# Kernel tuning notes

Hardware: AMD Instinct MI355X
Metric: run time of the kernel (lower is better)

Reference implementation:

```python
import jax, jax.numpy as jnp
import numpy as np

NUM_HEADS = 8
DIM_HEAD = 64
SCALE = DIM_HEAD * NUM_HEADS  # q *= dim_head * num_heads, as in the source


def setup_inputs() -> dict:
    key = jax.random.key(0)
    k1, k2, k3, k4 = jax.random.split(key, 4)
    B, C, H, W = 8, 64, 32, 32
    x = jax.random.normal(k1, (B, C, H, W), dtype=jnp.float32)
    # 1x1 conv == matmul over channels; small init keeps post-scale logits sane
    w_qkv = jax.random.normal(k2, (3 * NUM_HEADS * DIM_HEAD, C), dtype=jnp.float32) * 0.02
    rel_h = jax.random.normal(k3, (2 * H - 1, DIM_HEAD), dtype=jnp.float32) * 0.02
    rel_w = jax.random.normal(k4, (2 * W - 1, DIM_HEAD), dtype=jnp.float32) * 0.02
    return {"x": x, "w_qkv": w_qkv, "rel_h": rel_h, "rel_w": rel_w}


def _rel_indices(H, W):
    # flattened 2D grid positions
    pos_y = np.repeat(np.arange(H), W)  # [HW]
    pos_x = np.tile(np.arange(W), H)    # [HW]
    rel_y = pos_y[None, :] - pos_y[:, None] + (H - 1)  # [HW, HW] in [0, 2H-2]
    rel_x = pos_x[None, :] - pos_x[:, None] + (W - 1)  # [HW, HW] in [0, 2W-2]
    return jnp.asarray(rel_y), jnp.asarray(rel_x)


def reference(x, w_qkv, rel_h, rel_w):
    B, C, H, W = x.shape
    n = H * W
    # 1x1 conv (bias=False) -> per-pixel matmul
    xf = x.reshape(B, C, n)                              # b c n
    qkv = jnp.einsum('oc,bcn->bon', w_qkv, xf)           # b (3 h d) n
    q, k, v = jnp.split(qkv, 3, axis=1)
    def to_heads(t):  # b (h d) n -> b h n d
        return t.reshape(B, NUM_HEADS, DIM_HEAD, n).transpose(0, 1, 3, 2)
    q, k, v = to_heads(q), to_heads(k), to_heads(v)
    q = q * SCALE  # scale applied before QK^T AND before pos bias (in-place in torch)

    sim = jnp.einsum('bhid,bhjd->bhij', q, k)            # [B, h, n, n]

    # relative position bias: q_i . rel_h[dy] + q_i . rel_w[dx]
    logits_h = jnp.einsum('bhid,rd->bhir', q, rel_h)     # [B, h, n, 2H-1]
    logits_w = jnp.einsum('bhid,rd->bhir', q, rel_w)     # [B, h, n, 2W-1]
    rel_y, rel_x = _rel_indices(H, W)                    # [n, n] each
    i_idx = jnp.arange(n)[:, None]                       # [n, 1]
    bias = logits_h[:, :, i_idx, rel_y] + logits_w[:, :, i_idx, rel_x]  # [B,h,n,n]

    attn = jax.nn.softmax(sim + bias, axis=-1)
    out = jnp.einsum('bhij,bhjd->bhid', attn, v)         # [B, h, n, d]
    out = out.transpose(0, 1, 3, 2).reshape(B, NUM_HEADS * DIM_HEAD, H, W)
    return out
```

## Files before the change

kernel.cpp:

```cpp
#include <hip/hip_runtime.h>
#include <hip/hip_bf16.h>
#include <hip/hip_fp16.h>

typedef _Float16 h8 __attribute__((ext_vector_type(8)));
typedef _Float16 h2 __attribute__((ext_vector_type(2)));
typedef unsigned short us8 __attribute__((ext_vector_type(8)));
typedef float f4 __attribute__((ext_vector_type(4)));
typedef float f16v __attribute__((ext_vector_type(16)));
typedef int i2v __attribute__((ext_vector_type(2)));

#define NH 8
#define DH 64
#define NPIX 1024
#define CIN 64
#define NBH 64
#define QSCALE (512.0f * 1.44269504f)
#define LOSCALE 2048.0f
#define INV_LOSCALE (1.0f / 2048.0f)
#define DTHR 12.0f

__device__ __forceinline__ void gload_lds16(const void* g, void* lds) {
  __builtin_amdgcn_global_load_lds(
      (const __attribute__((address_space(1))) void*)g,
      (__attribute__((address_space(3))) void*)lds, 16, 0, 0);
// ... 84 lines not shown
  f4 zf = {0.f, 0.f, 0.f, 0.f};
  f4 acc[2][4], cor[2][4];
  #pragma unroll
  for (int oi = 0; oi < 2; ++oi)
    #pragma unroll
    for (int pi = 0; pi < 4; ++pi) { acc[oi][pi] = zf; cor[oi][pi] = zf; }

  const int ob = w * 32;
  #pragma unroll
  for (int kh = 0; kh < 2; ++kh) {
    h8 ah[2], al[2], bh[4], bl[4];
    #pragma unroll
    for (int oi = 0; oi < 2; ++oi) {
      int orow = ob + ((c >> 2) << 3) + (c & 3) + oi * 4;
      int ch = (((kh * 4 + g) ^ (orow & 7)) << 4);
      ah[oi] = *(const h8*)(Wh + orow * 128 + ch);
      al[oi] = *(const h8*)(Wl + orow * 128 + ch);
    }
    #pragma unroll
    for (int pi = 0; pi < 4; ++pi) {
      int prow = pi * 16 + c;
      int ch = (((kh * 4 + g) ^ (prow & 7)) << 4);
      bh[pi] = *(const h8*)(Xh + prow * 128 + ch);
      bl[pi] = *(const h8*)(Xl + prow * 128 + ch);
    }
    __builtin_amdgcn_s_setprio(1);
    #pragma unroll
    for (int oi = 0; oi < 2; ++oi)
      #pragma unroll
      for (int pi = 0; pi < 4; ++pi) {
        acc[oi][pi] = __builtin_amdgcn_mfma_f32_16x16x32_f16(ah[oi], bh[pi], acc[oi][pi], 0, 0, 0);
        cor[oi][pi] = __builtin_amdgcn_mfma_f32_16x16x32_f16(ah[oi], bl[pi], cor[oi][pi], 0, 0, 0);
        cor[oi][pi] = __builtin_amdgcn_mfma_f32_16x16x32_f16(al[oi], bh[pi], cor[oi][pi], 0, 0, 0);
      }
    __builtin_amdgcn_s_setprio(0);
  }

  const int part = o0 >> 9;
  const float scl = part == 0 ? QSCALE : 1.0f;
  _Float16* dsth = part == 0 ? Qh : (part == 1 ? Kh : Vv);
  _Float16* dstl = part == 0 ? Ql : (part == 1 ? Kl : nullptr);

  __syncthreads();
  {
    const int chunk = 4 * w + g;
    #pragma unroll
    for (int pi = 0; pi < 4; ++pi) {
      int p = pi * 16 + c;
      h8 hv, lv;
      #pragma unroll
      for (int oi = 0; oi < 2; ++oi)
        #pragma unroll
        for (int reg = 0; reg < 4; ++reg) {
          float v = (acc[oi][pi][reg] + cor[oi][pi][reg] * INV_LOSCALE) * scl;
          _Float16 hh = (_Float16)v;
          hv[oi * 4 + reg] = hh;
          lv[oi * 4 + reg] = (_Float16)(v - (float)hh);
        }
      int byo = p * 256 + ((chunk ^ (p & 15)) << 4);
      *(h8*)(Thi + byo) = hv;
      if (dstl) *(h8*)(Tlo + byo) = lv;
    }
  }
  __syncthreads();
  #pragma unroll
  for (int it = 0; it < 4; ++it) {
    int task = tid + it * 256;
    int p = task >> 4;
    int ck = task & 15;
    int byo = p * 256 + ((ck ^ (p & 15)) << 4);
    int o = o0 + ck * 8;
    int h = (o >> 6) & 7;
    int d = o & 63;
    size_t off = (((size_t)(b * NH + h)) * NPIX + p0 + p) * DH + d;
    h8 v = *(const h8*)(Thi + byo);
    *(h8*)(dsth + off) = v;
    if (dstl) {
      h8 v2 = *(const h8*)(Tlo + byo);
      *(h8*)(dstl + off) = v2;
    }
  }
}

__global__ __launch_bounds__(256, 2) void attn_mfma(
    const _Float16* __restrict__ Qh, const _Float16* __restrict__ Ql,
    const _Float16* __restrict__ Kh, const _Float16* __restrict__ Kl,
    const _Float16* __restrict__ V,
    const float* __restrict__ rel_h, const float* __restrict__ rel_w,
    float* __restrict__ out) {
  __shared__ __align__(16) char SMem[57344];
  _Float16* LHc = (_Float16*)(SMem + 49152);
  _Float16* LWT = (_Float16*)(SMem + 32768);
  float* OT = (float*)SMem;

  const int tid = threadIdx.x;
  const int lane = tid & 63;
  const int w = tid >> 6;
  const int wu = __builtin_amdgcn_readfirstlane(w);
  const int c = lane & 15;
  const int g = lane >> 4;
  const int il = lane & 31;
  const int hi = lane >> 5;
  const int bx = blockIdx.x;
  const int bh = ((bx & 7) << 3) | ((bx >> 3) & 7);
  const int i0 = (bx >> 6) << 7;

  const _Float16* Qhg = Qh + (size_t)bh * NPIX * DH;
  const _Float16* Qlg = Ql + (size_t)bh * NPIX * DH;
  const _Float16* Khg = Kh + (size_t)bh * NPIX * DH;
  const _Float16* Klg = Kl + (size_t)bh * NPIX * DH;
  const _Float16* Vg  = V  + (size_t)bh * NPIX * DH;

  const h8* Qr0h = (const h8*)(Qhg + (size_t)(i0 + w * 32 + c) * DH);
  const h8* Qr0l = (const h8*)(Qlg + (size_t)(i0 + w * 32 + c) * DH);
  const h8* Qr1h = (const h8*)(Qhg + (size_t)(i0 + w * 32 + 16 + c) * DH);
  const h8* Qr1l = (const h8*)(Qlg + (size_t)(i0 + w * 32 + 16 + c) * DH);
  h8 q0h[2] = {Qr0h[g], Qr0h[4 + g]};
  h8 q0l[2] = {Qr0l[g], Qr0l[4 + g]};
  h8 q1h[2] = {Qr1h[g], Qr1h[4 + g]};
  h8 q1l[2] = {Qr1l[g], Qr1l[4 + g]};

  const int s0i = wu * 128 + lane;
  const int s1i = s0i + 64;
  const int ko0 = (s0i >> 3) * 128 + (((s0i & 7) ^ ((s0i >> 3) & 7)) << 4);
  const int ko1 = (s1i >> 3) * 128 + (((s1i & 7) ^ ((s1i >> 3) & 7)) << 4);

  #pragma unroll
  for (int it = 0; it < 2; ++it) {
    int task = tid + it * 256;
    int oct = task & 7, s = task >> 3;
    int ss = s < 63 ? s : 62;
    const float* sh = rel_h + (size_t)ss * DH + oct * 8;
    const float* sw = rel_w + (size_t)ss * DH + oct * 8;
    h8 hh, ww;
    #pragma unroll
    for (int e = 0; e < 8; ++e) {
      hh[e] = (_Float16)sh[e];
      ww[e] = (_Float16)sw[e];
    }
    int byo = s * 128 + ((oct ^ (s & 7)) << 4);
    *(h8*)(SMem + byo) = hh;
    *(h8*)(SMem + 16384 + byo) = ww;
  }
  __syncthreads();

  const int yi = (i0 + w * 32) >> 5;
  f4 zf = {0.f, 0.f, 0.f, 0.f};
  #pragma unroll
  for (int rs = 0; rs < 2; ++rs) {
    f4 lhD[4], lwD[4];
    #pragma unroll
    for (int st = 0; st < 4; ++st) { lhD[st] = zf; lwD[st] = zf; }
    #pragma unroll
    for (int kh = 0; kh < 2; ++kh) {
      h8 bq = rs ? q1h[kh] : q0h[kh];
      h8 bl = rs ? q1l[kh] : q0l[kh];
      #pragma unroll
      for (int st = 0; st < 4; ++st) {
        int srow = st * 16 + c;
        int chb = srow * 128 + (((kh * 4 + g) ^ (srow & 7)) << 4);
        h8 ra = *(const h8*)(SMem + chb);
        h8 wa = *(const h8*)(SMem + 16384 + chb);
        lhD[st] = __builtin_amdgcn_mfma_f32_16x16x32_f16(ra, bq, lhD[st], 0, 0, 0);
        lhD[st] = __builtin_amdgcn_mfma_f32_16x16x32_f16(ra, bl, lhD[st], 0, 0, 0);
        lwD[st] = __builtin_amdgcn_mfma_f32_16x16x32_f16(wa, bq, lwD[st], 0, 0, 0);
        lwD[st] = __builtin_amdgcn_mfma_f32_16x16x32_f16(wa, bl, lwD[st], 0, 0, 0);
      }
    }
    int lrow = w * 32 + rs * 16 + c;
    #pragma unroll
    for (int st = 0; st < 4; ++st)
      #pragma unroll
      for (int reg = 0; reg < 4; ++reg) {
        int s = st * 16 + 4 * g + reg;
        int k = s - 31 + yi;
        if (k >= 0 && k < 32)
          LHc[(k >> 1) * 256 + lrow * 2 + (k & 1)] = (_Float16)lhD[st][reg];
        LWT[lrow * 64 + s] = (_Float16)lwD[st][reg];
      }
  }
  __syncthreads();

  float lwp[16];
  {
    int r = w * 32 + il;
    #pragma unroll
    for (int reg = 0; reg < 16; ++reg) {
      int jl = (reg & 3) + 8 * (reg >> 2) + 4 * hi;
      lwp[reg] = (float)LWT[r * 64 + 31 + jl - il];
    }
  }
  const h8* Qmh = (const h8*)(Qhg + (size_t)(i0 + w * 32 + il) * DH);
  const h8* Qml = (const h8*)(Qlg + (size_t)(i0 + w * 32 + il) * DH);
  h8 qmh[4], qml[4];
  #pragma unroll
  for (int kb = 0; kb < 4; ++kb) {
    qmh[kb] = Qmh[2 * kb + hi];
    qml[kb] = Qml[2 * kb + hi];
  }
  __syncthreads();

  {
    gload_lds16((const char*)Khg + ko0, SMem + wu * 2048);
    gload_lds16((const char*)Khg + ko1, SMem + wu * 2048 + 1024);
    gload_lds16((const char*)Klg + ko0, SMem + 16384 + wu * 2048);
    gload_lds16((const char*)Klg + ko1, SMem + 16384 + wu * 2048 + 1024);
    int jp = tid & 31, dd = tid >> 5;
    const h8* vr = (const h8*)(Vg + (size_t)(2 * jp) * DH);
    h8 v0 = vr[dd], v1 = vr[8 + dd];
    us8 u0 = *(const us8*)&v0, u1 = *(const us8*)&v1;
    #pragma unroll
    for (int e = 0; e < 8; ++e) {
      int d = dd * 8 + e;
      unsigned int val = (unsigned int)u0[e] | ((unsigned int)u1[e] << 16);
      *(unsigned int*)(SMem + 32768 + d * 128 + (((jp >> 2) ^ (d & 7)) << 4) + (jp & 3) * 4) = val;
    }
  }
  __syncthreads();

  float m_s = -1e30f, lp = 0.f;
  f16v O0, O1;
  #pragma unroll
  for (int e = 0; e < 16; ++e) { O0[e] = 0.f; O1[e] = 0.f; }

  const int swl = (il & 7);
  int cur = 0;
  #pragma unroll 1
  for (int t = 0; t < 16; ++t) {
    char* Kc  = SMem + cur * 8192;
    char* KLc = SMem + 16384 + cur * 8192;
    char* Vc  = SMem + 32768 + cur * 8192;
    const int nxt = cur ^ 1;
    const bool pre = t < 15;
    const int jp = tid & 31, dd = tid >> 5;
    h8 v0 = {}, v1 = {};
    if (pre) {
      const char* kg  = (const char*)Khg + (size_t)(t + 1) * 8192;
      const char* klg = (const char*)Klg + (size_t)(t + 1) * 8192;
      gload_lds16(kg + ko0, SMem + nxt * 8192 + wu * 2048);
      gload_lds16(kg + ko1, SMem + nxt * 8192 + wu * 2048 + 1024);
      gload_lds16(klg + ko0, SMem + 16384 + nxt * 8192 + wu * 2048);
      gload_lds16(klg + ko1, SMem + 16384 + nxt * 8192 + wu * 2048 + 1024);
      const h8* vr = (const h8*)(Vg + (size_t)((t + 1) * 64 + 2 * jp) * DH);
      v0 = vr[dd];
      v1 = vr[8 + dd];
    }

    f16v S0, S1;
    #pragma unroll
    for (int e = 0; e < 16; ++e) { S0[e] = 0.f; S1[e] = 0.f; }
    #pragma unroll
    for (int kb = 0; kb < 4; ++kb) {
      int chb0 = il * 128 + (((2 * kb + hi) ^ swl) << 4);
      int chb1 = chb0 + 32 * 128;
      h8 a0h = *(const h8*)(Kc + chb0);
      h8 a0l = *(const h8*)(KLc + chb0);
      h8 a1h = *(const h8*)(Kc + chb1);
      h8 a1l = *(const h8*)(KLc + chb1);
      __builtin_amdgcn_s_setprio(1);
      S0 = __builtin_amdgcn_mfma_f32_32x32x16_f16(a0h, qmh[kb], S0, 0, 0, 0);
      S0 = __builtin_amdgcn_mfma_f32_32x32x16_f16(a0l, qmh[kb], S0, 0, 0, 0);
      S0 = __builtin_amdgcn_mfma_f32_32x32x16_f16(a0h, qml[kb], S0, 0, 0, 0);
      S1 = __builtin_amdgcn_mfma_f32_32x32x16_f16(a1h, qmh[kb], S1, 0, 0, 0);
      S1 = __builtin_amdgcn_mfma_f32_32x32x16_f16(a1l, qmh[kb], S1, 0, 0, 0);
      S1 = __builtin_amdgcn_mfma_f32_32x32x16_f16(a1h, qml[kb], S1, 0, 0, 0);
      __builtin_amdgcn_s_setprio(0);
    }

    h8 fr[4];
    {
      int r = w * 32 + il;
      h2 lhu = *(const h2*)(LHc + t * 256 + r * 2);
      float lh0 = (float)lhu[0], lh1 = (float)lhu[1];
      #pragma unroll
      for (int reg = 0; reg < 16; ++reg) {
        S0[reg] += lwp[reg] + lh0;
        S1[reg] += lwp[reg] + lh1;
      }
      float v8[8];
      #pragma unroll
      for (int e = 0; e < 8; ++e)
        v8[e] = fmaxf(fmaxf(S0[e], S0[e + 8]), fmaxf(S1[e], S1[e + 8]));
      float w0 = fmaxf(fmaxf(v8[0], v8[1]), fmaxf(v8[2], v8[3]));
      float w1 = fmaxf(fmaxf(v8[4], v8[5]), fmaxf(v8[6], v8[7]));
      float mx = fmaxf(w0, w1);
      mx = fmaxf(mx, __shfl_xor(mx, 32, 64));
      bool sk = mx <= m_s + DTHR;
      if (!__all(sk)) {
        float mn = fmaxf(m_s, mx);
        float corr = fexp2(m_s - mn);
        m_s = mn;
        lp *= corr;
        #pragma unroll
        for (int e = 0; e < 16; ++e) { O0[e] *= corr; O1[e] *= corr; }
      }
      float pv0[16], pv1[16];
      float sum = 0.f;
      #pragma unroll
      for (int e = 0; e < 16; ++e) {
        pv0[e] = fexp2(S0[e] - m_s);
        pv1[e] = fexp2(S1[e] - m_s);
        sum += pv0[e] + pv1[e];
      }
      lp += sum;
      #pragma unroll
      for (int jkb = 0; jkb < 4; ++jkb) {
        const float* pv = (jkb < 2) ? pv0 : pv1;
        int base = (jkb & 1) * 8;
        unsigned x01 = pk16(pv[base + 0], pv[base + 1]);
        unsigned x23 = pk16(pv[base + 2], pv[base + 3]);
        unsigned y01 = pk16(pv[base + 4], pv[base + 5]);
        unsigned y23 = pk16(pv[base + 6], pv[base + 7]);
        i2v r1 = __builtin_amdgcn_permlane32_swap((int)x01, (int)y01, false, false);
        i2v r2 = __builtin_amdgcn_permlane32_swap((int)x23, (int)y23, false, false);
        union { unsigned u[4]; h8 h; } fu;
        fu.u[0] = (unsigned)r1[0];
        fu.u[1] = (unsigned)r2[0];
        fu.u[2] = (unsigned)r1[1];
        fu.u[3] = (unsigned)r2[1];
        fr[jkb] = fu.h;
      }
    }

    #pragma unroll
    for (int jkb = 0; jkb < 4; ++jkb) {
      int och = (((2 * jkb + hi) ^ swl) << 4);
      __builtin_amdgcn_s_setprio(1);
      h8 av0 = *(const h8*)(Vc + il * 128 + och);
      h8 av1 = *(const h8*)(Vc + (32 + il) * 128 + och);
      O0 = __builtin_amdgcn_mfma_f32_32x32x16_f16(av0, fr[jkb], O0, 0, 0, 0);
      O1 = __builtin_amdgcn_mfma_f32_32x32x16_f16(av1, fr[jkb], O1, 0, 0, 0);
      __builtin_amdgcn_s_setprio(0);
    }

    if (pre) {
      us8 u0 = *(const us8*)&v0, u1 = *(const us8*)&v1;
      char* Vn = SMem + 32768 + nxt * 8192;
      #pragma unroll
      for (int e = 0; e < 8; ++e) {
        int d = dd * 8 + e;
        unsigned int val = (unsigned int)u0[e] | ((unsigned int)u1[e] << 16);
        *(unsigned int*)(Vn + d * 128 + (((jp >> 2) ^ (d & 7)) << 4) + (jp & 3) * 4) = val;
      }
    }
    __syncthreads();
    cur = nxt;
  }

  float lt = lp + __shfl_xor(lp, 32, 64);
  float rr = __builtin_amdgcn_rcpf(lt);
  {
    int r = w * 32 + il;
    #pragma unroll
    for (int reg = 0; reg < 16; ++reg) {
      int dl = (reg & 3) + 8 * (reg >> 2) + 4 * hi;
      int d0 = dl;
      int d1 = 32 + dl;
      OT[d0 * 128 + (r ^ ((d0 & 7) << 3))] = O0[reg] * rr;
      OT[d1 * 128 + (r ^ ((d1 & 7) << 3))] = O1[reg] * rr;
    }
  }
  __syncthreads();
  #pragma unroll
  for (int it = 0; it < 8; ++it) {
    int task = tid + it * 256;
    int rq = task & 31, d = task >> 5;
    f4 vv = *(const f4*)&OT[d * 128 + ((rq * 4) ^ ((d & 7) << 3))];
    *(f4*)(out + (((size_t)bh * 64 + d) << 10) + i0 + rq * 4) = vv;
  }
}

extern "C" void kernel_launch(void* const* d_in, const int* in_sizes, int n_in,
                              void* d_out, int out_size, void* d_ws, size_t ws_size,
                              hipStream_t stream) {
  const float* x  = (const float*)d_in[0];
  const float* wq = (const float*)d_in[1];
  const float* rh = (const float*)d_in[2];
  const float* rw = (const float*)d_in[3];
  float* out = (float*)d_out;

  const size_t sz = (size_t)NBH * NPIX * DH;
  _Float16* Qh = (_Float16*)d_ws;
  _Float16* Ql = Qh + sz;
  _Float16* Kh = Ql + sz;
  _Float16* Kl = Kh + sz;
  _Float16* V  = Kl + sz;

  qkv_mfma<<<dim3(12, 16, 8), 256, 0, stream>>>(x, wq, Qh, Ql, Kh, Kl, V);
  attn_mfma<<<dim3(512), 256, 0, stream>>>(Qh, Ql, Kh, Kl, V, rh, rw, out);
}
```

Baseline: 72.10 us.

## Software-pipeline QK^T of next tile with softmax and PV of current tile

Restructures the attention main loop into a two-stage software pipeline. The QK^T MFMAs for tile t+1 are issued before the softmax and PV of tile t, using two sets of score accumulators (SA/SB) and a loop unrolled by two over explicit named LDS buffers. This lets MFMA work overlap the exp/max/pack ALU work. The prologue now prefetches two K tiles, the V register prefetch is held in persistent registers, and the row-sum reduction uses four partial sums. The extra 32 accumulator registers per lane raise register pressure under launch_bounds(256,2), which risks spills or lower occupancy.

Result: slower. 73.68 us (+2.2%).

```diff
diff --git a/kernel.cpp b/kernel.cpp
--- a/kernel.cpp
+++ b/kernel.cpp
@@ -200,6 +200,12 @@
   _Float16* LHc = (_Float16*)(SMem + 49152);
   _Float16* LWT = (_Float16*)(SMem + 32768);
   float* OT = (float*)SMem;
+  char* kb0 = SMem;
+  char* kb1 = SMem + 8192;
+  char* klb0 = SMem + 16384;
+  char* klb1 = SMem + 24576;
+  char* vb0 = SMem + 32768;
+  char* vb1 = SMem + 40960;
 
   const int tid = threadIdx.x;
   const int lane = tid & 63;
@@ -209,9 +215,11 @@
   const int g = lane >> 4;
   const int il = lane & 31;
   const int hi = lane >> 5;
+  const int jp = tid & 31, dd = tid >> 5;
   const int bx = blockIdx.x;
   const int bh = ((bx & 7) << 3) | ((bx >> 3) & 7);
   const int i0 = (bx >> 6) << 7;
+  const int swl = (il & 7);
 
   const _Float16* Qhg = Qh + (size_t)bh * NPIX * DH;
   const _Float16* Qlg = Ql + (size_t)bh * NPIX * DH;
@@ -308,55 +316,15 @@
   }
   __syncthreads();
 
-  {
-    gload_lds16((const char*)Khg + ko0, SMem + wu * 2048);
-    gload_lds16((const char*)Khg + ko1, SMem + wu * 2048 + 1024);
-    gload_lds16((const char*)Klg + ko0, SMem + 16384 + wu * 2048);
-    gload_lds16((const char*)Klg + ko1, SMem + 16384 + wu * 2048 + 1024);
-    int jp = tid & 31, dd = tid >> 5;
-    const h8* vr = (const h8*)(Vg + (size_t)(2 * jp) * DH);
-    h8 v0 = vr[dd], v1 = vr[8 + dd];
-    us8 u0 = *(const us8*)&v0, u1 = *(const us8*)&v1;
-    #pragma unroll
-    for (int e = 0; e < 8; ++e) {
-      int d = dd * 8 + e;
-      unsigned int val = (unsigned int)u0[e] | ((unsigned int)u1[e] << 16);
-      *(unsigned int*)(SMem + 32768 + d * 128 + (((jp >> 2) ^ (d & 7)) << 4) + (jp & 3) * 4) = val;
-    }
-  }
-  __syncthreads();
-
   float m_s = -1e30f, lp = 0.f;
-  f16v O0, O1;
+  f16v O0, O1, SA0, SA1, SB0, SB1;
   #pragma unroll
   for (int e = 0; e < 16; ++e) { O0[e] = 0.f; O1[e] = 0.f; }
-
-  const int swl = (il & 7);
-  int cur = 0;
-  #pragma unroll 1
-  for (int t = 0; t < 16; ++t) {
-    char* Kc  = SMem + cur * 8192;
-    char* KLc = SMem + 16384 + cur * 8192;
-    char* Vc  = SMem + 32768 + cur * 8192;
-    const int nxt = cur ^ 1;
-    const bool pre = t < 15;
-    const int jp = tid & 31, dd = tid >> 5;
-    h8 v0 = {}, v1 = {};
-    if (pre) {
-      const char* kg  = (const char*)Khg + (size_t)(t + 1) * 8192;
-      const char* klg = (const char*)Klg + (size_t)(t + 1) * 8192;
-      gload_lds16(kg + ko0, SMem + nxt * 8192 + wu * 2048);
-      gload_lds16(kg + ko1, SMem + nxt * 8192 + wu * 2048 + 1024);
-      gload_lds16(klg + ko0, SMem + 16384 + nxt * 8192 + wu * 2048);
-      gload_lds16(klg + ko1, SMem + 16384 + nxt * 8192 + wu * 2048 + 1024);
-      const h8* vr = (const h8*)(Vg + (size_t)((t + 1) * 64 + 2 * jp) * DH);
-      v0 = vr[dd];
-      v1 = vr[8 + dd];
-    }
-
-    f16v S0, S1;
-    #pragma unroll
-    for (int e = 0; e < 16; ++e) { S0[e] = 0.f; S1[e] = 0.f; }
+  h8 vr0, vr1;
+
+  auto qk = [&](const char* Kc, const char* KLc, f16v& T0, f16v& T1) {
+    #pragma unroll
+    for (int e = 0; e < 16; ++e) { T0[e] = 0.f; T1[e] = 0.f; }
     #pragma unroll
     for (int kb = 0; kb < 4; ++kb) {
       int chb0 = il * 128 + (((2 * kb + hi) ^ swl) << 4);
@@ -366,70 +334,77 @@
       h8 a1h = *(const h8*)(Kc + chb1);
       h8 a1l = *(const h8*)(KLc + chb1);
       __builtin_amdgcn_s_setprio(1);
-      S0 = __builtin_amdgcn_mfma_f32_32x32x16_f16(a0h, qmh[kb], S0, 0, 0, 0);
-      S0 = __builtin_amdgcn_mfma_f32_32x32x16_f16(a0l, qmh[kb], S0, 0, 0, 0);
-      S0 = __builtin_amdgcn_mfma_f32_32x32x16_f16(a0h, qml[kb], S0, 0, 0, 0);
-      S1 = __builtin_amdgcn_mfma_f32_32x32x16_f16(a1h, qmh[kb], S1, 0, 0, 0);
-      S1 = __builtin_amdgcn_mfma_f32_32x32x16_f16(a1l, qmh[kb], S1, 0, 0, 0);
-      S1 = __builtin_amdgcn_mfma_f32_32x32x16_f16(a1h, qml[kb], S1, 0, 0, 0);
+      T0 = __builtin_amdgcn_mfma_f32_32x32x16_f16(a0h, qmh[kb], T0, 0, 0, 0);
+      T0 = __builtin_amdgcn_mfma_f32_32x32x16_f16(a0l, qmh[kb], T0, 0, 0, 0);
+      T0 = __builtin_amdgcn_mfma_f32_32x32x16_f16(a0h, qml[kb], T0, 0, 0, 0);
+      T1 = __builtin_amdgcn_mfma_f32_32x32x16_f16(a1h, qmh[kb], T1, 0, 0, 0);
+      T1 = __builtin_amdgcn_mfma_f32_32x32x16_f16(a1l, qmh[kb], T1, 0, 0, 0);
+      T1 = __builtin_amdgcn_mfma_f32_32x32x16_f16(a1h, qml[kb], T1, 0, 0, 0);
       __builtin_amdgcn_s_setprio(0);
     }
-
-    h8 fr[4];
-    {
-      int r = w * 32 + il;
-      h2 lhu = *(const h2*)(LHc + t * 256 + r * 2);
-      float lh0 = (float)lhu[0], lh1 = (float)lhu[1];
+  };
+
+  auto finish = [&](int t, f16v& S0, f16v& S1, h8* fr) {
+    int r = w * 32 + il;
+    h2 lhu = *(const h2*)(LHc + t * 256 + r * 2);
+    float lh0 = (float)lhu[0], lh1 = (float)lhu[1];
+    #pragma unroll
+    for (int reg = 0; reg < 16; ++reg) {
+      S0[reg] += lwp[reg] + lh0;
+      S1[reg] += lwp[reg] + lh1;
+    }
+    float v8[8];
+    #pragma unroll
+    for (int e = 0; e < 8; ++e)
+      v8[e] = fmaxf(fmaxf(S0[e], S0[e + 8]), fmaxf(S1[e], S1[e + 8]));
+    float w0 = fmaxf(fmaxf(v8[0], v8[1]), fmaxf(v8[2], v8[3]));
+    float w1 = fmaxf(fmaxf(v8[4], v8[5]), fmaxf(v8[6], v8[7]));
+    float mx = fmaxf(w0, w1);
+    mx = fmaxf(mx, __shfl_xor(mx, 32, 64));
+    bool sk = mx <= m_s + DTHR;
+    if (!__all(sk)) {
+      float mn = fmaxf(m_s, mx);
+      float corr = fexp2(m_s - mn);
+      m_s = mn;
+      lp *= corr;
       #pragma unroll
-      for (int reg = 0; reg < 16; ++reg) {
-        S0[reg] += lwp[reg] + lh0;
-        S1[reg] += lwp[reg] + lh1;
-      }
-      float v8[8];
-      #pragma unroll
-      for (int e = 0; e < 8; ++e)
-        v8[e] = fmaxf(fmaxf(S0[e], S0[e + 8]), fmaxf(S1[e], S1[e + 8]));
-      float w0 = fmaxf(fmaxf(v8[0], v8[1]), fmaxf(v8[2], v8[3]));
-      float w1 = fmaxf(fmaxf(v8[4], v8[5]), fmaxf(v8[6], v8[7]));
-      float mx = fmaxf(w0, w1);
-      mx = fmaxf(mx, __shfl_xor(mx, 32, 64));
-      bool sk = mx <= m_s + DTHR;
-      if (!__all(sk)) {
-        float mn = fmaxf(m_s, mx);
-        float corr = fexp2(m_s - mn);
-        m_s = mn;
-        lp *= corr;
-        #pragma unroll
-        for (int e = 0; e < 16; ++e) { O0[e] *= corr; O1[e] *= corr; }
-      }
-      float pv0[16], pv1[16];
-      float sum = 0.f;
-      #pragma unroll
-      for (int e = 0; e < 16; ++e) {
-        pv0[e] = fexp2(S0[e] - m_s);
-        pv1[e] = fexp2(S1[e] - m_s);
-        sum += pv0[e] + pv1[e];
-      }
-      lp += sum;
-      #pragma unroll
-      for (int jkb = 0; jkb < 4; ++jkb) {
-        const float* pv = (jkb < 2) ? pv0 : pv1;
-        int base = (jkb & 1) * 8;
-        unsigned x01 = pk16(pv[base + 0], pv[base + 1]);
-        unsigned x23 = pk16(pv[base + 2], pv[base + 3]);
-        unsigned y01 = pk16(pv[base + 4], pv[base + 5]);
-        unsigned y23 = pk16(pv[base + 6], pv[base + 7]);
-        i2v r1 = __builtin_amdgcn_permlane32_swap((int)x01, (int)y01, false, false);
-        i2v r2 = __builtin_amdgcn_permlane32_swap((int)x23, (int)y23, false, false);
-        union { unsigned u[4]; h8 h; } fu;
-        fu.u[0] = (unsigned)r1[0];
-        fu.u[1] = (unsigned)r2[0];
-        fu.u[2] = (unsigned)r1[1];
-        fu.u[3] = (unsigned)r2[1];
-        fr[jkb] = fu.h;
-      }
-    }
-
+      for (int e = 0; e < 16; ++e) { O0[e] *= corr; O1[e] *= corr; }
+    }
+    float pv0[16], pv1[16];
+    #pragma unroll
+    for (int e = 0; e < 16; ++e) {
+      pv0[e] = fexp2(S0[e] - m_s);
+      pv1[e] = fexp2(S1[e] - m_s);
+    }
+    f4 ps = zf;
+    #pragma unroll
+    for (int e = 0; e < 16; e += 4) {
+      ps[0] += pv0[e] + pv1[e];
+      ps[1] += pv0[e + 1] + pv1[e + 1];
+      ps[2] += pv0[e + 2] + pv1[e + 2];
+      ps[3] += pv0[e + 3] + pv1[e + 3];
+    }
+    lp += (ps[0] + ps[1]) + (ps[2] + ps[3]);
+    #pragma unroll
+    for (int jkb = 0; jkb < 4; ++jkb) {
+      const float* pv = (jkb < 2) ? pv0 : pv1;
+      int base = (jkb & 1) * 8;
+      unsigned x01 = pk16(pv[base + 0], pv[base + 1]);
+      unsigned x23 = pk16(pv[base + 2], pv[base + 3]);
+      unsigned y01 = pk16(pv[base + 4], pv[base + 5]);
+      unsigned y23 = pk16(pv[base + 6], pv[base + 7]);
+      i2v r1 = __builtin_amdgcn_permlane32_swap((int)x01, (int)y01, false, false);
+      i2v r2 = __builtin_amdgcn_permlane32_swap((int)x23, (int)y23, false, false);
+      union { unsigned u[4]; h8 h; } fu;
+      fu.u[0] = (unsigned)r1[0];
+      fu.u[1] = (unsigned)r2[0];
+      fu.u[2] = (unsigned)r1[1];
+      fu.u[3] = (unsigned)r2[1];
+      fr[jkb] = fu.h;
+    }
+  };
+
+  auto pv_step = [&](const char* Vc, const h8* fr) {
     #pragma unroll
     for (int jkb = 0; jkb < 4; ++jkb) {
       int och = (((2 * jkb + hi) ^ swl) << 4);
@@ -440,19 +415,87 @@
       O1 = __builtin_amdgcn_mfma_f32_32x32x16_f16(av1, fr[jkb], O1, 0, 0, 0);
       __builtin_amdgcn_s_setprio(0);
     }
-
-    if (pre) {
-      us8 u0 = *(const us8*)&v0, u1 = *(const us8*)&v1;
-      char* Vn = SMem + 32768 + nxt * 8192;
-      #pragma unroll
-      for (int e = 0; e < 8; ++e) {
-        int d = dd * 8 + e;
-        unsigned int val = (unsigned int)u0[e] | ((unsigned int)u1[e] << 16);
-        *(unsigned int*)(Vn + d * 128 + (((jp >> 2) ^ (d & 7)) << 4) + (jp & 3) * 4) = val;
-      }
-    }
-    __syncthreads();
-    cur = nxt;
+  };
+
+  auto vwrite = [&](char* vb) {
+    us8 u0 = *(const us8*)&vr0, u1 = *(const us8*)&vr1;
+    #pragma unroll
+    for (int e = 0; e < 8; ++e) {
+      int d = dd * 8 + e;
+      unsigned val = (unsigned)u0[e] | ((unsigned)u1[e] << 16);
+      *(unsigned*)(vb + d * 128 + (((jp >> 2) ^ (d & 7)) << 4) + (jp & 3) * 4) = val;
+    }
+  };
+
+  {
+    gload_lds16((const char*)Khg + ko0, kb0 + wu * 2048);
+    gload_lds16((const char*)Khg + ko1, kb0 + wu * 2048 + 1024);
+    gload_lds16((const char*)Klg + ko0, klb0 + wu * 2048);
+    gload_lds16((const char*)Klg + ko1, klb0 + wu * 2048 + 1024);
+    gload_lds16((const char*)Khg + 8192 + ko0, kb1 + wu * 2048);
+    gload_lds16((const char*)Khg + 8192 + ko1, kb1 + wu * 2048 + 1024);
+    gload_lds16((const char*)Klg + 8192 + ko0, klb1 + wu * 2048);
+    gload_lds16((const char*)Klg + 8192 + ko1, klb1 + wu * 2048 + 1024);
+    const h8* vrp = (const h8*)(Vg + (size_t)(2 * jp) * DH);
+    vr0 = vrp[dd];
+    vr1 = vrp[8 + dd];
+  }
+  __syncthreads();
+  vwrite(vb0);
+  {
+    const h8* vrp = (const h8*)(Vg + (size_t)(64 + 2 * jp) * DH);
+    vr0 = vrp[dd];
+    vr1 = vrp[8 + dd];
+  }
+  qk(kb0, klb0, SA0, SA1);
+  __syncthreads();
+
+  #pragma unroll 1
+  for (int tp = 0; tp < 8; ++tp) {
+    {
+      const int t = 2 * tp;
+      if (t < 14) {
+        const char* kg  = (const char*)Khg + (size_t)(t + 2) * 8192;
+        const char* klg = (const char*)Klg + (size_t)(t + 2) * 8192;
+        gload_lds16(kg + ko0, kb0 + wu * 2048);
+        gload_lds16(kg + ko1, kb0 + wu * 2048 + 1024);
+        gload_lds16(klg + ko0, klb0 + wu * 2048);
+        gload_lds16(klg + ko1, klb0 + wu * 2048 + 1024);
+      }
+      if (t < 15) vwrite(vb1);
+      if (t < 14) {
+        const h8* vrp = (const h8*)(Vg + (size_t)((t + 2) * 64 + 2 * jp) * DH);
+        vr0 = vrp[dd];
+        vr1 = vrp[8 + dd];
+      }
+      if (t < 15) qk(kb1, klb1, SB0, SB1);
+      h8 fr[4];
+      finish(t, SA0, SA1, fr);
+      pv_step(vb0, fr);
+      __syncthreads();
+    }
+    {
+      const int t = 2 * tp + 1;
+      if (t < 14) {
+        const char* kg  = (const char*)Khg + (size_t)(t + 2) * 8192;
+        const char* klg = (const char*)Klg + (size_t)(t + 2) * 8192;
+        gload_lds16(kg + ko0, kb1 + wu * 2048);
+        gload_lds16(kg + ko1, kb1 + wu * 2048 + 1024);
+        gload_lds16(klg + ko0, klb1 + wu * 2048);
+        gload_lds16(klg + ko1, klb1 + wu * 2048 + 1024);
+      }
+      if (t < 15) vwrite(vb0);
+      if (t < 14) {
+        const h8* vrp = (const h8*)(Vg + (size_t)((t + 2) * 64 + 2 * jp) * DH);
+        vr0 = vrp[dd];
+        vr1 = vrp[8 + dd];
+      }
+      if (t < 15) qk(kb0, klb0, SA0, SA1);
+      h8 fr[4];
+      finish(t, SB0, SB1, fr);
+      pv_step(vb1, fr);
+      __syncthreads();
+    }
   }
 
   float lt = lp + __shfl_xor(lp, 32, 64);
```

## Keep row-bias terms in registers, shrink LDS, raise occupancy, unroll KV loop

Applied to the files above, without the earlier changes.

The per-row height-bias values move out of a dedicated LDS region and into 16 packed registers per lane, loaded once before the main loop. LDS per block drops from 56 KB to 48 KB and the launch bound rises to 3 blocks per CU. The 16-step key/value loop is fully unrolled so buffer offsets become compile-time constants, and the row-sum reduction is split into four partial accumulators. More waves can hide memory latency, but the register budget at 3 blocks per CU is tighter, so the compiler may spill.

Result: no change. 71.76 us (-0.5%).

```diff
diff --git a/kernel.cpp b/kernel.cpp
--- a/kernel.cpp
+++ b/kernel.cpp
@@ -190,15 +190,15 @@
   }
 }
 
-__global__ __launch_bounds__(256, 2) void attn_mfma(
+__global__ __launch_bounds__(256, 3) void attn_mfma(
     const _Float16* __restrict__ Qh, const _Float16* __restrict__ Ql,
     const _Float16* __restrict__ Kh, const _Float16* __restrict__ Kl,
     const _Float16* __restrict__ V,
     const float* __restrict__ rel_h, const float* __restrict__ rel_w,
     float* __restrict__ out) {
-  __shared__ __align__(16) char SMem[57344];
-  _Float16* LHc = (_Float16*)(SMem + 49152);
-  _Float16* LWT = (_Float16*)(SMem + 32768);
+  __shared__ __align__(16) char SMem[49152];
+  _Float16* LWT = (_Float16*)SMem;
+  _Float16* LHt = (_Float16*)(SMem + 16384);
   float* OT = (float*)SMem;
 
   const int tid = threadIdx.x;
@@ -209,9 +209,11 @@
   const int g = lane >> 4;
   const int il = lane & 31;
   const int hi = lane >> 5;
+  const int jp = tid & 31, dd = tid >> 5;
   const int bx = blockIdx.x;
   const int bh = ((bx & 7) << 3) | ((bx >> 3) & 7);
   const int i0 = (bx >> 6) << 7;
+  const int swl = (il & 7);
 
   const _Float16* Qhg = Qh + (size_t)bh * NPIX * DH;
   const _Float16* Qlg = Ql + (size_t)bh * NPIX * DH;
@@ -247,8 +249,8 @@
       ww[e] = (_Float16)sw[e];
     }
     int byo = s * 128 + ((oct ^ (s & 7)) << 4);
-    *(h8*)(SMem + byo) = hh;
-    *(h8*)(SMem + 16384 + byo) = ww;
+    *(h8*)(SMem + 32768 + byo) = hh;
+    *(h8*)(SMem + 40960 + byo) = ww;
   }
   __syncthreads();
 
@@ -267,8 +269,8 @@
       for (int st = 0; st < 4; ++st) {
         int srow = st * 16 + c;
         int chb = srow * 128 + (((kh * 4 + g) ^ (srow & 7)) << 4);
-        h8 ra = *(const h8*)(SMem + chb);
-        h8 wa = *(const h8*)(SMem + 16384 + chb);
+        h8 ra = *(const h8*)(SMem + 32768 + chb);
+        h8 wa = *(const h8*)(SMem + 40960 + chb);
         lhD[st] = __builtin_amdgcn_mfma_f32_16x16x32_f16(ra, bq, lhD[st], 0, 0, 0);
         lhD[st] = __builtin_amdgcn_mfma_f32_16x16x32_f16(ra, bl, lhD[st], 0, 0, 0);
         lwD[st] = __builtin_amdgcn_mfma_f32_16x16x32_f16(wa, bq, lwD[st], 0, 0, 0);
@@ -282,14 +284,14 @@
       for (int reg = 0; reg < 4; ++reg) {
         int s = st * 16 + 4 * g + reg;
         int k = s - 31 + yi;
-        if (k >= 0 && k < 32)
-          LHc[(k >> 1) * 256 + lrow * 2 + (k & 1)] = (_Float16)lhD[st][reg];
+        if (k >= 0 && k < 32) LHt[lrow * 32 + k] = (_Float16)lhD[st][reg];
         LWT[lrow * 64 + s] = (_Float16)lwD[st][reg];
       }
   }
   __syncthreads();
 
   float lwp[16];
+  unsigned lhreg[16];
   {
     int r = w * 32 + il;
     #pragma unroll
@@ -297,6 +299,9 @@
       int jl = (reg & 3) + 8 * (reg >> 2) + 4 * hi;
       lwp[reg] = (float)LWT[r * 64 + 31 + jl - il];
     }
+    #pragma unroll
+    for (int t = 0; t < 16; ++t)
+      lhreg[t] = *(const unsigned*)(LHt + r * 32 + 2 * t);
   }
   const h8* Qmh = (const h8*)(Qhg + (size_t)(i0 + w * 32 + il) * DH);
   const h8* Qml = (const h8*)(Qlg + (size_t)(i0 + w * 32 + il) * DH);
@@ -313,15 +318,14 @@
     gload_lds16((const char*)Khg + ko1, SMem + wu * 2048 + 1024);
     gload_lds16((const char*)Klg + ko0, SMem + 16384 + wu * 2048);
     gload_lds16((const char*)Klg + ko1, SMem + 16384 + wu * 2048 + 1024);
-    int jp = tid & 31, dd = tid >> 5;
     const h8* vr = (const h8*)(Vg + (size_t)(2 * jp) * DH);
     h8 v0 = vr[dd], v1 = vr[8 + dd];
     us8 u0 = *(const us8*)&v0, u1 = *(const us8*)&v1;
     #pragma unroll
     for (int e = 0; e < 8; ++e) {
       int d = dd * 8 + e;
-      unsigned int val = (unsigned int)u0[e] | ((unsigned int)u1[e] << 16);
-      *(unsigned int*)(SMem + 32768 + d * 128 + (((jp >> 2) ^ (d & 7)) << 4) + (jp & 3) * 4) = val;
+      unsigned val = (unsigned)u0[e] | ((unsigned)u1[e] << 16);
+      *(unsigned*)(SMem + 32768 + d * 128 + (((jp >> 2) ^ (d & 7)) << 4) + (jp & 3) * 4) = val;
     }
   }
   __syncthreads();
@@ -331,24 +335,22 @@
   #pragma unroll
   for (int e = 0; e < 16; ++e) { O0[e] = 0.f; O1[e] = 0.f; }
 
-  const int swl = (il & 7);
-  int cur = 0;
-  #pragma unroll 1
+  #pragma unroll
   for (int t = 0; t < 16; ++t) {
-    char* Kc  = SMem + cur * 8192;
-    char* KLc = SMem + 16384 + cur * 8192;
-    char* Vc  = SMem + 32768 + cur * 8192;
-    const int nxt = cur ^ 1;
-    const bool pre = t < 15;
-    const int jp = tid & 31, dd = tid >> 5;
+    char* Kc  = SMem + (t & 1) * 8192;
+    char* KLc = SMem + 16384 + (t & 1) * 8192;
+    char* Vc  = SMem + 32768 + (t & 1) * 8192;
+    char* Kn  = SMem + ((t + 1) & 1) * 8192;
+    char* KLn = SMem + 16384 + ((t + 1) & 1) * 8192;
+    char* Vn  = SMem + 32768 + ((t + 1) & 1) * 8192;
     h8 v0 = {}, v1 = {};
-    if (pre) {
+    if (t < 15) {
       const char* kg  = (const char*)Khg + (size_t)(t + 1) * 8192;
       const char* klg = (const char*)Klg + (size_t)(t + 1) * 8192;
-      gload_lds16(kg + ko0, SMem + nxt * 8192 + wu * 2048);
-      gload_lds16(kg + ko1, SMem + nxt * 8192 + wu * 2048 + 1024);
-      gload_lds16(klg + ko0, SMem + 16384 + nxt * 8192 + wu * 2048);
-      gload_lds16(klg + ko1, SMem + 16384 + nxt * 8192 + wu * 2048 + 1024);
+      gload_lds16(kg + ko0, Kn + wu * 2048);
+      gload_lds16(kg + ko1, Kn + wu * 2048 + 1024);
+      gload_lds16(klg + ko0, KLn + wu * 2048);
+      gload_lds16(klg + ko1, KLn + wu * 2048 + 1024);
       const h8* vr = (const h8*)(Vg + (size_t)((t + 1) * 64 + 2 * jp) * DH);
       v0 = vr[dd];
       v1 = vr[8 + dd];
@@ -377,9 +379,9 @@
 
     h8 fr[4];
     {
-      int r = w * 32 + il;
-      h2 lhu = *(const h2*)(LHc + t * 256 + r * 2);
-      float lh0 = (float)lhu[0], lh1 = (float)lhu[1];
+      union { unsigned u; h2 h; } lu;
+      lu.u = lhreg[t];
+      float lh0 = (float)lu.h[0], lh1 = (float)lu.h[1];
       #pragma unroll
       for (int reg = 0; reg < 16; ++reg) {
         S0[reg] += lwp[reg] + lh0;
@@ -403,14 +405,20 @@
         for (int e = 0; e < 16; ++e) { O0[e] *= corr; O1[e] *= corr; }
       }
       float pv0[16], pv1[16];
-      float sum = 0.f;
       #pragma unroll
       for (int e = 0; e < 16; ++e) {
         pv0[e] = fexp2(S0[e] - m_s);
         pv1[e] = fexp2(S1[e] - m_s);
-        sum += pv0[e] + pv1[e];
-      }
-      lp += sum;
+      }
+      f4 ps = zf;
+      #pragma unroll
+      for (int e = 0; e < 16; e += 4) {
+        ps[0] += pv0[e] + pv1[e];
+        ps[1] += pv0[e + 1] + pv1[e + 1];
+        ps[2] += pv0[e + 2] + pv1[e + 2];
+        ps[3] += pv0[e + 3] + pv1[e + 3];
+      }
+      lp += (ps[0] + ps[1]) + (ps[2] + ps[3]);
       #pragma unroll
       for (int jkb = 0; jkb < 4; ++jkb) {
         const float* pv = (jkb < 2) ? pv0 : pv1;
@@ -441,18 +449,16 @@
       __builtin_amdgcn_s_setprio(0);
     }
 
-    if (pre) {
+    if (t < 15) {
       us8 u0 = *(const us8*)&v0, u1 = *(const us8*)&v1;
-      char* Vn = SMem + 32768 + nxt * 8192;
       #pragma unroll
       for (int e = 0; e < 8; ++e) {
         int d = dd * 8 + e;
-        unsigned int val = (unsigned int)u0[e] | ((unsigned int)u1[e] << 16);
-        *(unsigned int*)(Vn + d * 128 + (((jp >> 2) ^ (d & 7)) << 4) + (jp & 3) * 4) = val;
+        unsigned val = (unsigned)u0[e] | ((unsigned)u1[e] << 16);
+        *(unsigned*)(Vn + d * 128 + (((jp >> 2) ^ (d & 7)) << 4) + (jp & 3) * 4) = val;
       }
     }
     __syncthreads();
-    cur = nxt;
   }
 
   float lt = lp + __shfl_xor(lp, 32, 64);
```

## Split key loop across two wave groups per block and merge softmax partials

Applied to the files above, without the earlier changes.

Doubles the attention block to 512 threads and splits the 16 key/value tiles between two groups of four waves, each keeping its own online-softmax state. The partial max, sum and output accumulators are exchanged through shared memory and merged at the end. Each group now single-buffers its K/V tiles with extra barriers instead of double-buffering. This aims to raise wave occupancy and halve the serial loop length, at the cost of more synchronisation, a merge step and less load/compute overlap per group.

Measured after the change: 80.30 us. +11.4%, slower.

```diff
diff --git a/kernel.cpp b/kernel.cpp
--- a/kernel.cpp
+++ b/kernel.cpp
@@ -190,7 +190,7 @@
   }
 }
 
-__global__ __launch_bounds__(256, 2) void attn_mfma(
+__global__ __launch_bounds__(512) void attn_mfma(
     const _Float16* __restrict__ Qh, const _Float16* __restrict__ Ql,
     const _Float16* __restrict__ Kh, const _Float16* __restrict__ Kl,
     const _Float16* __restrict__ V,
@@ -199,19 +199,28 @@
   __shared__ __align__(16) char SMem[57344];
   _Float16* LHc = (_Float16*)(SMem + 49152);
   _Float16* LWT = (_Float16*)(SMem + 32768);
+  float* EX = (float*)SMem;
   float* OT = (float*)SMem;
 
   const int tid = threadIdx.x;
   const int lane = tid & 63;
-  const int w = tid >> 6;
-  const int wu = __builtin_amdgcn_readfirstlane(w);
+  const int wu = tid >> 6;
+  const int lw = wu & 3;
+  const int grp = wu >> 2;
   const int c = lane & 15;
   const int g = lane >> 4;
   const int il = lane & 31;
   const int hi = lane >> 5;
+  const int gtid = tid & 255;
+  const int jp = gtid & 31, dd = gtid >> 5;
   const int bx = blockIdx.x;
   const int bh = ((bx & 7) << 3) | ((bx >> 3) & 7);
   const int i0 = (bx >> 6) << 7;
+  const int swl = (il & 7);
+
+  char* KHb = SMem + grp * 8192;
+  char* KLb = SMem + 16384 + grp * 8192;
+  char* VBb = SMem + 32768 + grp * 8192;
 
   const _Float16* Qhg = Qh + (size_t)bh * NPIX * DH;
   const _Float16* Qlg = Ql + (size_t)bh * NPIX * DH;
@@ -219,24 +228,13 @@
   const _Float16* Klg = Kl + (size_t)bh * NPIX * DH;
   const _Float16* Vg  = V  + (size_t)bh * NPIX * DH;
 
-  const h8* Qr0h = (const h8*)(Qhg + (size_t)(i0 + w * 32 + c) * DH);
-  const h8* Qr0l = (const h8*)(Qlg + (size_t)(i0 + w * 32 + c) * DH);
-  const h8* Qr1h = (const h8*)(Qhg + (size_t)(i0 + w * 32 + 16 + c) * DH);
-  const h8* Qr1l = (const h8*)(Qlg + (size_t)(i0 + w * 32 + 16 + c) * DH);
-  h8 q0h[2] = {Qr0h[g], Qr0h[4 + g]};
-  h8 q0l[2] = {Qr0l[g], Qr0l[4 + g]};
-  h8 q1h[2] = {Qr1h[g], Qr1h[4 + g]};
-  h8 q1l[2] = {Qr1l[g], Qr1l[4 + g]};
-
-  const int s0i = wu * 128 + lane;
+  const int s0i = lw * 128 + lane;
   const int s1i = s0i + 64;
   const int ko0 = (s0i >> 3) * 128 + (((s0i & 7) ^ ((s0i >> 3) & 7)) << 4);
   const int ko1 = (s1i >> 3) * 128 + (((s1i & 7) ^ ((s1i >> 3) & 7)) << 4);
 
-  #pragma unroll
-  for (int it = 0; it < 2; ++it) {
-    int task = tid + it * 256;
-    int oct = task & 7, s = task >> 3;
+  {
+    int oct = tid & 7, s = tid >> 3;
     int ss = s < 63 ? s : 62;
     const float* sh = rel_h + (size_t)ss * DH + oct * 8;
     const float* sw = rel_w + (size_t)ss * DH + oct * 8;
@@ -252,54 +250,64 @@
   }
   __syncthreads();
 
-  const int yi = (i0 + w * 32) >> 5;
   f4 zf = {0.f, 0.f, 0.f, 0.f};
-  #pragma unroll
-  for (int rs = 0; rs < 2; ++rs) {
-    f4 lhD[4], lwD[4];
-    #pragma unroll
-    for (int st = 0; st < 4; ++st) { lhD[st] = zf; lwD[st] = zf; }
-    #pragma unroll
-    for (int kh = 0; kh < 2; ++kh) {
-      h8 bq = rs ? q1h[kh] : q0h[kh];
-      h8 bl = rs ? q1l[kh] : q0l[kh];
-      #pragma unroll
-      for (int st = 0; st < 4; ++st) {
-        int srow = st * 16 + c;
-        int chb = srow * 128 + (((kh * 4 + g) ^ (srow & 7)) << 4);
-        h8 ra = *(const h8*)(SMem + chb);
-        h8 wa = *(const h8*)(SMem + 16384 + chb);
-        lhD[st] = __builtin_amdgcn_mfma_f32_16x16x32_f16(ra, bq, lhD[st], 0, 0, 0);
-        lhD[st] = __builtin_amdgcn_mfma_f32_16x16x32_f16(ra, bl, lhD[st], 0, 0, 0);
-        lwD[st] = __builtin_amdgcn_mfma_f32_16x16x32_f16(wa, bq, lwD[st], 0, 0, 0);
-        lwD[st] = __builtin_amdgcn_mfma_f32_16x16x32_f16(wa, bl, lwD[st], 0, 0, 0);
-      }
-    }
-    int lrow = w * 32 + rs * 16 + c;
-    #pragma unroll
-    for (int st = 0; st < 4; ++st)
-      #pragma unroll
-      for (int reg = 0; reg < 4; ++reg) {
-        int s = st * 16 + 4 * g + reg;
-        int k = s - 31 + yi;
-        if (k >= 0 && k < 32)
-          LHc[(k >> 1) * 256 + lrow * 2 + (k & 1)] = (_Float16)lhD[st][reg];
-        LWT[lrow * 64 + s] = (_Float16)lwD[st][reg];
-      }
+  if (grp == 0) {
+    const h8* Qr0h = (const h8*)(Qhg + (size_t)(i0 + lw * 32 + c) * DH);
+    const h8* Qr0l = (const h8*)(Qlg + (size_t)(i0 + lw * 32 + c) * DH);
+    const h8* Qr1h = (const h8*)(Qhg + (size_t)(i0 + lw * 32 + 16 + c) * DH);
+    const h8* Qr1l = (const h8*)(Qlg + (size_t)(i0 + lw * 32 + 16 + c) * DH);
+    h8 q0h[2] = {Qr0h[g], Qr0h[4 + g]};
+    h8 q0l[2] = {Qr0l[g], Qr0l[4 + g]};
+    h8 q1h[2] = {Qr1h[g], Qr1h[4 + g]};
+    h8 q1l[2] = {Qr1l[g], Qr1l[4 + g]};
+    const int yi = (i0 + lw * 32) >> 5;
+    #pragma unroll
+    for (int rs = 0; rs < 2; ++rs) {
+      f4 lhD[4], lwD[4];
+      #pragma unroll
+      for (int st = 0; st < 4; ++st) { lhD[st] = zf; lwD[st] = zf; }
+      #pragma unroll
+      for (int kh = 0; kh < 2; ++kh) {
+        h8 bq = rs ? q1h[kh] : q0h[kh];
+        h8 bl = rs ? q1l[kh] : q0l[kh];
+        #pragma unroll
+        for (int st = 0; st < 4; ++st) {
+          int srow = st * 16 + c;
+          int chb = srow * 128 + (((kh * 4 + g) ^ (srow & 7)) << 4);
+          h8 ra = *(const h8*)(SMem + chb);
+          h8 wa = *(const h8*)(SMem + 16384 + chb);
+          lhD[st] = __builtin_amdgcn_mfma_f32_16x16x32_f16(ra, bq, lhD[st], 0, 0, 0);
+          lhD[st] = __builtin_amdgcn_mfma_f32_16x16x32_f16(ra, bl, lhD[st], 0, 0, 0);
+          lwD[st] = __builtin_amdgcn_mfma_f32_16x16x32_f16(wa, bq, lwD[st], 0, 0, 0);
+          lwD[st] = __builtin_amdgcn_mfma_f32_16x16x32_f16(wa, bl, lwD[st], 0, 0, 0);
+        }
+      }
+      int lrow = lw * 32 + rs * 16 + c;
+      #pragma unroll
+      for (int st = 0; st < 4; ++st)
+        #pragma unroll
+        for (int reg = 0; reg < 4; ++reg) {
+          int s = st * 16 + 4 * g + reg;
+          int k = s - 31 + yi;
+          if (k >= 0 && k < 32)
+            LHc[(k >> 1) * 256 + lrow * 2 + (k & 1)] = (_Float16)lhD[st][reg];
+          LWT[lrow * 64 + s] = (_Float16)lwD[st][reg];
+        }
+    }
   }
   __syncthreads();
 
   float lwp[16];
   {
-    int r = w * 32 + il;
+    int r = lw * 32 + il;
     #pragma unroll
     for (int reg = 0; reg < 16; ++reg) {
       int jl = (reg & 3) + 8 * (reg >> 2) + 4 * hi;
       lwp[reg] = (float)LWT[r * 64 + 31 + jl - il];
     }
   }
-  const h8* Qmh = (const h8*)(Qhg + (size_t)(i0 + w * 32 + il) * DH);
-  const h8* Qml = (const h8*)(Qlg + (size_t)(i0 + w * 32 + il) * DH);
+  const h8* Qmh = (const h8*)(Qhg + (size_t)(i0 + lw * 32 + il) * DH);
+  const h8* Qml = (const h8*)(Qlg + (size_t)(i0 + lw * 32 + il) * DH);
   h8 qmh[4], qml[4];
   #pragma unroll
   for (int kb = 0; kb < 4; ++kb) {
@@ -308,20 +316,20 @@
   }
   __syncthreads();
 
-  {
-    gload_lds16((const char*)Khg + ko0, SMem + wu * 2048);
-    gload_lds16((const char*)Khg + ko1, SMem + wu * 2048 + 1024);
-    gload_lds16((const char*)Klg + ko0, SMem + 16384 + wu * 2048);
-    gload_lds16((const char*)Klg + ko1, SMem + 16384 + wu * 2048 + 1024);
-    int jp = tid & 31, dd = tid >> 5;
-    const h8* vr = (const h8*)(Vg + (size_t)(2 * jp) * DH);
+  const int tg0 = grp << 3;
+  {
+    gload_lds16((const char*)Khg + (size_t)tg0 * 8192 + ko0, KHb + lw * 2048);
+    gload_lds16((const char*)Khg + (size_t)tg0 * 8192 + ko1, KHb + lw * 2048 + 1024);
+    gload_lds16((const char*)Klg + (size_t)tg0 * 8192 + ko0, KLb + lw * 2048);
+    gload_lds16((const char*)Klg + (size_t)tg0 * 8192 + ko1, KLb + lw * 2048 + 1024);
+    const h8* vr = (const h8*)(Vg + (size_t)(tg0 * 64 + 2 * jp) * DH);
     h8 v0 = vr[dd], v1 = vr[8 + dd];
     us8 u0 = *(const us8*)&v0, u1 = *(const us8*)&v1;
     #pragma unroll
     for (int e = 0; e < 8; ++e) {
       int d = dd * 8 + e;
-      unsigned int val = (unsigned int)u0[e] | ((unsigned int)u1[e] << 16);
-      *(unsigned int*)(SMem + 32768 + d * 128 + (((jp >> 2) ^ (d & 7)) << 4) + (jp & 3) * 4) = val;
+      unsigned val = (unsigned)u0[e] | ((unsigned)u1[e] << 16);
+      *(unsigned*)(VBb + d * 128 + (((jp >> 2) ^ (d & 7)) << 4) + (jp & 3) * 4) = val;
     }
   }
   __syncthreads();
@@ -331,25 +339,13 @@
   #pragma unroll
   for (int e = 0; e < 16; ++e) { O0[e] = 0.f; O1[e] = 0.f; }
 
-  const int swl = (il & 7);
-  int cur = 0;
   #pragma unroll 1
-  for (int t = 0; t < 16; ++t) {
-    char* Kc  = SMem + cur * 8192;
-    char* KLc = SMem + 16384 + cur * 8192;
-    char* Vc  = SMem + 32768 + cur * 8192;
-    const int nxt = cur ^ 1;
-    const bool pre = t < 15;
-    const int jp = tid & 31, dd = tid >> 5;
+  for (int t = 0; t < 8; ++t) {
+    const int tg = tg0 + t;
+    const bool pre = t < 7;
     h8 v0 = {}, v1 = {};
     if (pre) {
-      const char* kg  = (const char*)Khg + (size_t)(t + 1) * 8192;
-      const char* klg = (const char*)Klg + (size_t)(t + 1) * 8192;
-      gload_lds16(kg + ko0, SMem + nxt * 8192 + wu * 2048);
-      gload_lds16(kg + ko1, SMem + nxt * 8192 + wu * 2048 + 1024);
-      gload_lds16(klg + ko0, SMem + 16384 + nxt * 8192 + wu * 2048);
-      gload_lds16(klg + ko1, SMem + 16384 + nxt * 8192 + wu * 2048 + 1024);
-      const h8* vr = (const h8*)(Vg + (size_t)((t + 1) * 64 + 2 * jp) * DH);
+      const h8* vr = (const h8*)(Vg + (size_t)((tg + 1) * 64 + 2 * jp) * DH);
       v0 = vr[dd];
       v1 = vr[8 + dd];
     }
@@ -361,10 +357,10 @@
     for (int kb = 0; kb < 4; ++kb) {
       int chb0 = il * 128 + (((2 * kb + hi) ^ swl) << 4);
       int chb1 = chb0 + 32 * 128;
-      h8 a0h = *(const h8*)(Kc + chb0);
-      h8 a0l = *(const h8*)(KLc + chb0);
-      h8 a1h = *(const h8*)(Kc + chb1);
-      h8 a1l = *(const h8*)(KLc + chb1);
+      h8 a0h = *(const h8*)(KHb + chb0);
+      h8 a0l = *(const h8*)(KLb + chb0);
+      h8 a1h = *(const h8*)(KHb + chb1);
+      h8 a1l = *(const h8*)(KLb + chb1);
       __builtin_amdgcn_s_setprio(1);
       S0 = __builtin_amdgcn_mfma_f32_32x32x16_f16(a0h, qmh[kb], S0, 0, 0, 0);
       S0 = __builtin_amdgcn_mfma_f32_32x32x16_f16(a0l, qmh[kb], S0, 0, 0, 0);
@@ -377,8 +373,8 @@
 
     h8 fr[4];
     {
-      int r = w * 32 + il;
-      h2 lhu = *(const h2*)(LHc + t * 256 + r * 2);
+      int r = lw * 32 + il;
+      h2 lhu = *(const h2*)(LHc + tg * 256 + r * 2);
       float lh0 = (float)lhu[0], lh1 = (float)lhu[1];
       #pragma unroll
       for (int reg = 0; reg < 16; ++reg) {
@@ -403,14 +399,20 @@
         for (int e = 0; e < 16; ++e) { O0[e] *= corr; O1[e] *= corr; }
       }
       float pv0[16], pv1[16];
-      float sum = 0.f;
       #pragma unroll
       for (int e = 0; e < 16; ++e) {
         pv0[e] = fexp2(S0[e] - m_s);
         pv1[e] = fexp2(S1[e] - m_s);
-        sum += pv0[e] + pv1[e];
-      }
-      lp += sum;
+      }
+      f4 ps = zf;
+      #pragma unroll
+      for (int e = 0; e < 16; e += 4) {
+        ps[0] += pv0[e] + pv1[e];
+        ps[1] += pv0[e + 1] + pv1[e + 1];
+        ps[2] += pv0[e + 2] + pv1[e + 2];
+        ps[3] += pv0[e + 3] + pv1[e + 3];
+      }
+      lp += (ps[0] + ps[1]) + (ps[2] + ps[3]);
       #pragma unroll
       for (int jkb = 0; jkb < 4; ++jkb) {
         const float* pv = (jkb < 2) ? pv0 : pv1;
@@ -429,49 +431,76 @@
         fr[jkb] = fu.h;
       }
     }
+    __syncthreads();
+    if (pre) {
+      const char* kg  = (const char*)Khg + (size_t)(tg + 1) * 8192;
+      const char* klg = (const char*)Klg + (size_t)(tg + 1) * 8192;
+      gload_lds16(kg + ko0, KHb + lw * 2048);
+      gload_lds16(kg + ko1, KHb + lw * 2048 + 1024);
+      gload_lds16(klg + ko0, KLb + lw * 2048);
+      gload_lds16(klg + ko1, KLb + lw * 2048 + 1024);
+    }
 
     #pragma unroll
     for (int jkb = 0; jkb < 4; ++jkb) {
       int och = (((2 * jkb + hi) ^ swl) << 4);
       __builtin_amdgcn_s_setprio(1);
-      h8 av0 = *(const h8*)(Vc + il * 128 + och);
-      h8 av1 = *(const h8*)(Vc + (32 + il) * 128 + och);
+      h8 av0 = *(const h8*)(VBb + il * 128 + och);
+      h8 av1 = *(const h8*)(VBb + (32 + il) * 128 + och);
       O0 = __builtin_amdgcn_mfma_f32_32x32x16_f16(av0, fr[jkb], O0, 0, 0, 0);
       O1 = __builtin_amdgcn_mfma_f32_32x32x16_f16(av1, fr[jkb], O1, 0, 0, 0);
       __builtin_amdgcn_s_setprio(0);
     }
-
+    __syncthreads();
     if (pre) {
       us8 u0 = *(const us8*)&v0, u1 = *(const us8*)&v1;
-      char* Vn = SMem + 32768 + nxt * 8192;
       #pragma unroll
       for (int e = 0; e < 8; ++e) {
         int d = dd * 8 + e;
-        unsigned int val = (unsigned int)u0[e] | ((unsigned int)u1[e] << 16);
-        *(unsigned int*)(Vn + d * 128 + (((jp >> 2) ^ (d & 7)) << 4) + (jp & 3) * 4) = val;
-      }
-    }
-    __syncthreads();
-    cur = nxt;
-  }
-
-  float lt = lp + __shfl_xor(lp, 32, 64);
-  float rr = __builtin_amdgcn_rcpf(lt);
-  {
-    int r = w * 32 + il;
+        unsigned val = (unsigned)u0[e] | ((unsigned)u1[e] << 16);
+        *(unsigned*)(VBb + d * 128 + (((jp >> 2) ^ (d & 7)) << 4) + (jp & 3) * 4) = val;
+      }
+    }
+  }
+
+  __syncthreads();
+  {
+    float* exw = EX + ((size_t)(wu * 64 + lane)) * 18;
+    exw[0] = m_s;
+    exw[1] = lp;
+    const f16v& Oout = grp ? O0 : O1;
+    #pragma unroll
+    for (int e = 0; e < 16; ++e) exw[2 + e] = Oout[e];
+  }
+  __syncthreads();
+  float rr;
+  f16v Om;
+  {
+    const float* exp_ = EX + ((size_t)((wu ^ 4) * 64 + lane)) * 18;
+    float pm = exp_[0], plp = exp_[1];
+    float M = fmaxf(m_s, pm);
+    float ca = fexp2(m_s - M);
+    float cb = fexp2(pm - M);
+    float Ll = lp * ca + plp * cb;
+    float L = Ll + __shfl_xor(Ll, 32, 64);
+    rr = __builtin_amdgcn_rcpf(L);
+    const f16v& Omy = grp ? O1 : O0;
+    #pragma unroll
+    for (int e = 0; e < 16; ++e) Om[e] = Omy[e] * ca + exp_[2 + e] * cb;
+  }
+  __syncthreads();
+  {
+    int r = lw * 32 + il;
     #pragma unroll
     for (int reg = 0; reg < 16; ++reg) {
-      int dl = (reg & 3) + 8 * (reg >> 2) + 4 * hi;
-      int d0 = dl;
-      int d1 = 32 + dl;
-      OT[d0 * 128 + (r ^ ((d0 & 7) << 3))] = O0[reg] * rr;
-      OT[d1 * 128 + (r ^ ((d1 & 7) << 3))] = O1[reg] * rr;
-    }
-  }
-  __syncthreads();
-  #pragma unroll
-  for (int it = 0; it < 8; ++it) {
-    int task = tid + it * 256;
+      int d = grp * 32 + (reg & 3) + 8 * (reg >> 2) + 4 * hi;
+      OT[d * 128 + (r ^ ((d & 7) << 3))] = Om[reg] * rr;
+    }
+  }
+  __syncthreads();
+  #pragma unroll
+  for (int it = 0; it < 4; ++it) {
+    int task = tid + it * 512;
     int rq = task & 31, d = task >> 5;
     f4 vv = *(const f4*)&OT[d * 128 + ((rq * 4) ^ ((d & 7) << 3))];
     *(f4*)(out + (((size_t)bh * 64 + d) << 10) + i0 + rq * 4) = vv;
@@ -495,5 +524,5 @@
   _Float16* V  = Kl + sz;
 
   qkv_mfma<<<dim3(12, 16, 8), 256, 0, stream>>>(x, wq, Qh, Ql, Kh, Kl, V);
-  attn_mfma<<<dim3(512), 256, 0, stream>>>(Qh, Ql, Kh, Kl, V, rh, rw, out);
+  attn_mfma<<<dim3(512), 512, 0, stream>>>(Qh, Ql, Kh, Kl, V, rh, rw, out);
 }
```
